# Optimization experiments

Measured on AMD Instinct MI355X. Metric: run time of the kernel, lower is better.

The kernel has to match this reference:

```python
import jax, jax.numpy as jnp
import numpy as np

N_NODES = 50000
N_EDGES = 800000
N_GRAPHS = 256
D_FEAT = 96
HIDDEN = 32


def setup_inputs() -> dict:
    key = jax.random.key(0)
    ks = jax.random.split(key, 8)
    x = jax.random.normal(ks[0], (N_NODES, D_FEAT), dtype=jnp.float32)
    edge_index = jax.random.randint(ks[1], (2, N_EDGES), 0, N_NODES, dtype=jnp.int64)
    batch = jnp.sort(jax.random.randint(ks[2], (N_NODES,), 0, N_GRAPHS, dtype=jnp.int64))
    W1 = jax.random.normal(ks[3], (D_FEAT, HIDDEN), dtype=jnp.float32) * 0.05
    b1 = jnp.zeros((HIDDEN,), dtype=jnp.float32)
    W2 = jax.random.normal(ks[4], (HIDDEN, HIDDEN), dtype=jnp.float32) * 0.05
    b2 = jnp.zeros((HIDDEN,), dtype=jnp.float32)
    Wc = jax.random.normal(ks[5], (HIDDEN, 2), dtype=jnp.float32) * 0.05
    bc = jnp.zeros((2,), dtype=jnp.float32)
    return {"x": x, "edge_index": edge_index, "batch": batch,
            "W1": W1, "b1": b1, "W2": W2, "b2": b2, "Wc": Wc, "bc": bc}


def reference(x, edge_index, batch, W1, b1, W2, b2, Wc, bc):
    src, dst = edge_index[0], edge_index[1]
    # GIN aggregation (eps=0): h_i = x_i + sum_{j -> i} x_j, scatter-add over edges
    agg = jax.ops.segment_sum(x[src], dst, num_segments=N_NODES)
    h = agg + x
    # 2-layer MLP inside GINConv
    h = jnp.maximum(h @ W1 + b1, 0.0) @ W2 + b2
    # outer ReLU (F.relu in forward)
    h = jnp.maximum(h, 0.0)
    # global mean pool per graph
    sums = jax.ops.segment_sum(h, batch, num_segments=N_GRAPHS)          # [G, H]
    counts = jax.ops.segment_sum(jnp.ones((N_NODES,), h.dtype), batch,
                                 num_segments=N_GRAPHS)                   # [G]
    pooled = sums / jnp.maximum(counts, 1.0)[:, None]
    return pooled @ Wc + bc  # [G, 2]
```

## Files before the change

kernel.cpp:

```cpp
#include <hip/hip_runtime.h>
#include <hip/hip_fp16.h>

#define N_NODES 50000
#define N_EDGES 800000
#define N_GRAPHS 256
#define D_FEAT 96
#define HIDDEN 32

#define NB 196
#define PB 500
#define PCHUNK 1600
#define SEGCAP 32
#define NLOAD 16
#define GWIN 16
#define LCAP 6400
#define XT 64
#define XBLK 782
#define XS_STRIDE 97
#define DUMMY_NODE N_NODES

__global__ void __launch_bounds__(256)
k_part(const int* __restrict__ src, const int* __restrict__ dst,
       unsigned int* __restrict__ binned, unsigned short* __restrict__ cnt) {
    __shared__ int hcur[NB];
    int blk = blockIdx.x;
    int tid = threadIdx.x;
    for (int i = tid; i < NB; i += 256) hcur[i] = 0;
    __syncthreads();

    int e0 = blk * PCHUNK, e1 = e0 + PCHUNK;
    for (int it = 0; it < PCHUNK; it += 1024) {
        int e = e0 + it + tid * 4;
        if (e < e1) {
            int4 s4 = *(const int4*)&src[e];
            int4 d4 = *(const int4*)&dst[e];
            unsigned w0 = (unsigned)s4.x | ((unsigned)(d4.x & 255) << 16);
            unsigned w1 = (unsigned)s4.y | ((unsigned)(d4.y & 255) << 16);
            unsigned w2 = (unsigned)s4.z | ((unsigned)(d4.z & 255) << 16);
            unsigned w3 = (unsigned)s4.w | ((unsigned)(d4.w & 255) << 16);
            int b0 = d4.x >> 8, b1 = d4.y >> 8, b2 = d4.z >> 8, b3 = d4.w >> 8;
            int p0 = atomicAdd(&hcur[b0], 1);
            int p1 = atomicAdd(&hcur[b1], 1);
            int p2 = atomicAdd(&hcur[b2], 1);
            int p3 = atomicAdd(&hcur[b3], 1);
            if (p0 < SEGCAP) binned[((size_t)b0 * PB + blk) * SEGCAP + p0] = w0;
            if (p1 < SEGCAP) binned[((size_t)b1 * PB + blk) * SEGCAP + p1] = w1;
            if (p2 < SEGCAP) binned[((size_t)b2 * PB + blk) * SEGCAP + p2] = w2;
            if (p3 < SEGCAP) binned[((size_t)b3 * PB + blk) * SEGCAP + p3] = w3;
        }
    }
    __syncthreads();

    for (int i = tid; i < NB; i += 256) {
        int c = hcur[i]; if (c > SEGCAP) c = SEGCAP;
        cnt[i * PB + blk] = (unsigned short)c;
    }
}

__global__ void __launch_bounds__(256)
k_x(const float* __restrict__ x, const float* __restrict__ W1,
    __half* __restrict__ y16, float* __restrict__ sums,
    float* __restrict__ counts) {
    __shared__ float xs[XT * XS_STRIDE];
    int xb = blockIdx.x;
    int tid = threadIdx.x;
    int n0 = xb * XT;
    int nn = N_NODES - n0; if (nn > XT) nn = XT;

    int gid = xb * 256 + tid;
    if (gid < N_GRAPHS * HIDDEN) sums[gid] = 0.f;
    if (gid < N_GRAPHS) counts[gid] = 0.f;
    if (xb == 0 && tid < HIDDEN)
        y16[(size_t)DUMMY_NODE * HIDDEN + tid] = __float2half(0.f);

    const float4* xsrc = (const float4*)(x + (size_t)n0 * D_FEAT);
    int nf4 = nn * (D_FEAT / 4);
    for (int idx = tid; idx < nf4; idx += 256) {
        int ln = (idx * 2731) >> 16;
        int k4 = idx - ln * 24;
        float4 v = xsrc[idx];
        float* dp = &xs[ln * XS_STRIDE + k4 * 4];
        dp[0] = v.x; dp[1] = v.y; dp[2] = v.z; dp[3] = v.w;
    }
    __syncthreads();

    int lane = tid & 63;
    int f0 = (tid >> 6) << 3;
    f0 = __builtin_amdgcn_readfirstlane(f0);

    if (lane < nn) {
        const float* xr = &xs[lane * XS_STRIDE];
        const float4* W1v = (const float4*)W1;
        float acc[8];
#pragma unroll
        for (int j = 0; j < 8; ++j) acc[j] = 0.f;
#pragma unroll
        for (int k = 0; k < D_FEAT; ++k) {
            float xv = xr[k];
            float4 wa = W1v[k * 8 + (f0 >> 2)];
            float4 wb = W1v[k * 8 + (f0 >> 2) + 1];
            acc[0] = fmaf(xv, wa.x, acc[0]);
            acc[1] = fmaf(xv, wa.y, acc[1]);
            acc[2] = fmaf(xv, wa.z, acc[2]);
            acc[3] = fmaf(xv, wa.w, acc[3]);
            acc[4] = fmaf(xv, wb.x, acc[4]);
            acc[5] = fmaf(xv, wb.y, acc[5]);
            acc[6] = fmaf(xv, wb.z, acc[6]);
            acc[7] = fmaf(xv, wb.w, acc[7]);
        }
        __half2 h01 = __floats2half2_rn(acc[0], acc[1]);
        __half2 h23 = __floats2half2_rn(acc[2], acc[3]);
        __half2 h45 = __floats2half2_rn(acc[4], acc[5]);
        __half2 h67 = __floats2half2_rn(acc[6], acc[7]);
        float4 pack;
        pack.x = __uint_as_float(*(const unsigned*)&h01);
        pack.y = __uint_as_float(*(const unsigned*)&h23);
        pack.z = __uint_as_float(*(const unsigned*)&h45);
        pack.w = __uint_as_float(*(const unsigned*)&h67);
        *(float4*)&y16[(size_t)(n0 + lane) * HIDDEN + f0] = pack;
    }
}

__global__ void __launch_bounds__(1024)
k_agg(const unsigned int* __restrict__ binned, const unsigned short* __restrict__ cnt,
      const __half* __restrict__ y16, const int* __restrict__ batch,
      const float* __restrict__ b1, const float* __restrict__ W2,
      const float* __restrict__ b2,
      float* __restrict__ sums, float* __restrict__ counts) {
    __shared__ unsigned int list[LCAP];
    __shared__ unsigned short list2[LCAP];
    __shared__ unsigned int sA[512], sB[512];
    __shared__ unsigned short cs[PB];
    __shared__ unsigned int sOfs[PB];
    __shared__ unsigned int ncnt[256];
    __shared__ unsigned int offs[257];
    __shared__ unsigned int cur[256];
    __shared__ float w2s[HIDDEN * HIDDEN];
    __shared__ float accs[GWIN * HIDDEN];
    __shared__ float cntsl[GWIN];

    int tid = threadIdx.x;
    int bin = blockIdx.x;
    if (tid < 256) ncnt[tid] = 0;
    w2s[tid] = W2[tid];
    if (tid < GWIN * HIDDEN) accs[tid] = 0.f;
    if (tid < GWIN) cntsl[tid] = 0.f;
    if (tid < 512) {
        unsigned c = (tid < PB) ? (unsigned)cnt[bin * PB + tid] : 0u;
        if (tid < PB) cs[tid] = (unsigned short)c;
        sA[tid] = c;
    }

    const unsigned int* ebase = binned + (size_t)bin * PB * SEGCAP;
    unsigned u[NLOAD];
#pragma unroll
    for (int j = 0; j < NLOAD; ++j)
        u[j] = ebase[tid + j * 1024];
    __syncthreads();

    unsigned *ps = sA, *pd = sB;
    for (int d = 1; d < 512; d <<= 1) {
        if (tid < 512) { unsigned v = ps[tid]; if (tid >= d) v += ps[tid - d]; pd[tid] = v; }
        __syncthreads();
        unsigned* t = ps; ps = pd; pd = t;
    }
    if (tid < PB) sOfs[tid] = tid ? ps[tid - 1] : 0u;
    int ecount = (int)ps[PB - 1];
    if (ecount > LCAP) ecount = LCAP;
    __syncthreads();

#pragma unroll
    for (int j = 0; j < NLOAD; ++j) {
        int idx = tid + j * 1024;
        if (idx < PB * SEGCAP) {
            int s = idx >> 5;
            int i = idx & 31;
            if (i < (int)cs[s]) {
                unsigned pos = sOfs[s] + i;
                if (pos < LCAP) list[pos] = u[j];
            }
        }
    }
    __syncthreads();

    for (int e = tid; e < ecount; e += 1024)
        atomicAdd(&ncnt[list[e] >> 16], 1u);
    __syncthreads();

    if (tid < 256) sA[tid] = (ncnt[tid] + 7u) & ~7u;
    __syncthreads();
    ps = sA; pd = sB;
    for (int d = 1; d < 256; d <<= 1) {
        if (tid < 256) { unsigned v = ps[tid]; if (tid >= d) v += ps[tid - d]; pd[tid] = v; }
        __syncthreads();
        unsigned* t = ps; ps = pd; pd = t;
    }
    if (tid < 256) {
        offs[tid + 1] = ps[tid];
        cur[tid] = tid ? ps[tid - 1] : 0u;
    }
    if (tid == 0) offs[0] = 0;
    __syncthreads();

    for (int e = tid; e < ecount; e += 1024) {
        unsigned p = list[e];
        unsigned pos = atomicAdd(&cur[p >> 16], 1u);
        if (pos < LCAP) list2[pos] = (unsigned short)(p & 0xFFFFu);
    }
    __syncthreads();
    if (tid < 256) {
        unsigned i0 = cur[tid], i1 = offs[tid + 1];
        for (unsigned i = i0; i < i1 && i < LCAP; ++i)
            list2[i] = (unsigned short)DUMMY_NODE;
    }
    __syncthreads();

    int node0 = bin << 8;
    int nn = N_NODES - node0; if (nn > 256) nn = 256;
    int g = tid >> 5;
    int f = tid & 31;
    int gfirst = batch[node0];

    for (int ln = g * 8; ln < g * 8 + 8; ++ln) {
        if (ln >= nn) break;
        int node = node0 + ln;
        float acc = __half2float(y16[(size_t)node * HIDDEN + f]);
        int j = offs[ln], jend = offs[ln + 1];
        for (; j < jend; j += 8) {
            ushort4 qa = *(const ushort4*)&list2[j];
            ushort4 qb = *(const ushort4*)&list2[j + 4];
            float a0 = __half2float(y16[(size_t)qa.x * HIDDEN + f]);
            float a1 = __half2float(y16[(size_t)qa.y * HIDDEN + f]);
            float a2 = __half2float(y16[(size_t)qa.z * HIDDEN + f]);
            float a3 = __half2float(y16[(size_t)qa.w * HIDDEN + f]);
            float a4 = __half2float(y16[(size_t)qb.x * HIDDEN + f]);
            float a5 = __half2float(y16[(size_t)qb.y * HIDDEN + f]);
            float a6 = __half2float(y16[(size_t)qb.z * HIDDEN + f]);
            float a7 = __half2float(y16[(size_t)qb.w * HIDDEN + f]);
            acc += ((a0 + a1) + (a2 + a3)) + ((a4 + a5) + (a6 + a7));
        }

        float h1 = fmaxf(acc + b1[f], 0.f);
        float h2 = b2[f];
#pragma unroll
        for (int k = 0; k < HIDDEN; ++k)
            h2 = fmaf(__shfl(h1, k, 32), w2s[k * HIDDEN + f], h2);
        float h = fmaxf(h2, 0.f);

        int gr = batch[node];
        int b = gr - gfirst;
        if (b < GWIN) {
            atomicAdd(&accs[b * HIDDEN + f], h);
            if (f == 0) atomicAdd(&cntsl[b], 1.f);
        } else {
            atomicAdd(&sums[(size_t)gr * HIDDEN + f], h);
            if (f == 0) atomicAdd(&counts[gr], 1.f);
        }
    }
    __syncthreads();

    for (int i = tid; i < GWIN * HIDDEN; i += 1024) {
        float v = accs[i];
        if (v != 0.f) atomicAdd(&sums[(size_t)gfirst * HIDDEN + i], v);
    }
    if (tid < GWIN) {
        float c = cntsl[tid];
        if (c != 0.f) atomicAdd(&counts[gfirst + tid], c);
    }
}

__global__ void k_out(const float* __restrict__ sums, const float* __restrict__ counts,
                      const float* __restrict__ Wc, const float* __restrict__ bc,
                      float* __restrict__ out) {
    int g = threadIdx.x;
    if (g >= N_GRAPHS) return;
    float inv = 1.f / fmaxf(counts[g], 1.f);
    float o0 = bc[0], o1 = bc[1];
#pragma unroll
    for (int k = 0; k < HIDDEN; ++k) {
        float p = sums[(size_t)g * HIDDEN + k] * inv;
        o0 = fmaf(p, Wc[k * 2 + 0], o0);
        o1 = fmaf(p, Wc[k * 2 + 1], o1);
    }
    out[g * 2 + 0] = o0;
    out[g * 2 + 1] = o1;
}

extern "C" void kernel_launch(void* const* d_in, const int* in_sizes, int n_in,
                              void* d_out, int out_size, void* d_ws, size_t ws_size,
                              hipStream_t stream) {
    const float* x     = (const float*)d_in[0];
    const int*   ei    = (const int*)d_in[1];
    const int*   batch = (const int*)d_in[2];
    const float* W1    = (const float*)d_in[3];
    const float* b1    = (const float*)d_in[4];
    const float* W2    = (const float*)d_in[5];
    const float* b2    = (const float*)d_in[6];
    const float* Wc    = (const float*)d_in[7];
    const float* bc    = (const float*)d_in[8];
    float* out = (float*)d_out;

    char* ws = (char*)d_ws;
    float*          sums   = (float*)ws;
    float*          counts = (float*)(ws + 32768);
    unsigned short* cnt    = (unsigned short*)(ws + 33792);
    unsigned int*   binned = (unsigned int*)(ws + 230400);
    __half*         y16    = (__half*)(ws + 12774400);

    k_part<<<PB, 256, 0, stream>>>(ei, ei + N_EDGES, binned, cnt);

    k_x<<<XBLK, 256, 0, stream>>>(x, W1, y16, sums, counts);

    k_agg<<<NB, 1024, 0, stream>>>(binned, cnt, y16, batch,
                                   b1, W2, b2, sums, counts);

    k_out<<<1, 256, 0, stream>>>(sums, counts, Wc, bc, out);
}
```

Baseline: 131.9 us.

## Merge partition and projection kernels; fold output head into aggregation via ticket

Fuses the edge-partitioning and node-projection kernels into one launch, with each block branching on its index to do one role, so both run concurrently. The final classifier kernel is removed: the last k_agg block to finish, detected through an atomic ticket after a threadfence, computes the pooled outputs. This cuts two kernel launches and lets the two independent front stages overlap. In exchange it adds a serialized tail on one block and a shared-memory union sized for the larger role.

```diff
diff --git a/kernel.cpp b/kernel.cpp
--- a/kernel.cpp
+++ b/kernel.cpp
@@ -20,104 +20,106 @@
 #define DUMMY_NODE N_NODES
 
 __global__ void __launch_bounds__(256)
-k_part(const int* __restrict__ src, const int* __restrict__ dst,
-       unsigned int* __restrict__ binned, unsigned short* __restrict__ cnt) {
-    __shared__ int hcur[NB];
+k_front(const float* __restrict__ x, const float* __restrict__ W1,
+        __half* __restrict__ y16,
+        const int* __restrict__ src, const int* __restrict__ dst,
+        unsigned int* __restrict__ binned, unsigned short* __restrict__ cnt,
+        float* __restrict__ sums, float* __restrict__ counts,
+        unsigned int* __restrict__ ticket) {
+    __shared__ __align__(16) char smem[26656];
     int blk = blockIdx.x;
     int tid = threadIdx.x;
-    for (int i = tid; i < NB; i += 256) hcur[i] = 0;
-    __syncthreads();
-
-    int e0 = blk * PCHUNK, e1 = e0 + PCHUNK;
-    for (int it = 0; it < PCHUNK; it += 1024) {
-        int e = e0 + it + tid * 4;
-        if (e < e1) {
-            int4 s4 = *(const int4*)&src[e];
-            int4 d4 = *(const int4*)&dst[e];
-            unsigned w0 = (unsigned)s4.x | ((unsigned)(d4.x & 255) << 16);
-            unsigned w1 = (unsigned)s4.y | ((unsigned)(d4.y & 255) << 16);
-            unsigned w2 = (unsigned)s4.z | ((unsigned)(d4.z & 255) << 16);
-            unsigned w3 = (unsigned)s4.w | ((unsigned)(d4.w & 255) << 16);
-            int b0 = d4.x >> 8, b1 = d4.y >> 8, b2 = d4.z >> 8, b3 = d4.w >> 8;
-            int p0 = atomicAdd(&hcur[b0], 1);
-            int p1 = atomicAdd(&hcur[b1], 1);
-            int p2 = atomicAdd(&hcur[b2], 1);
-            int p3 = atomicAdd(&hcur[b3], 1);
-            if (p0 < SEGCAP) binned[((size_t)b0 * PB + blk) * SEGCAP + p0] = w0;
-            if (p1 < SEGCAP) binned[((size_t)b1 * PB + blk) * SEGCAP + p1] = w1;
-            if (p2 < SEGCAP) binned[((size_t)b2 * PB + blk) * SEGCAP + p2] = w2;
-            if (p3 < SEGCAP) binned[((size_t)b3 * PB + blk) * SEGCAP + p3] = w3;
-        }
-    }
-    __syncthreads();
-
-    for (int i = tid; i < NB; i += 256) {
-        int c = hcur[i]; if (c > SEGCAP) c = SEGCAP;
-        cnt[i * PB + blk] = (unsigned short)c;
-    }
-}
-
-__global__ void __launch_bounds__(256)
-k_x(const float* __restrict__ x, const float* __restrict__ W1,
-    __half* __restrict__ y16, float* __restrict__ sums,
-    float* __restrict__ counts) {
-    __shared__ float xs[XT * XS_STRIDE];
-    int xb = blockIdx.x;
-    int tid = threadIdx.x;
-    int n0 = xb * XT;
-    int nn = N_NODES - n0; if (nn > XT) nn = XT;
-
-    int gid = xb * 256 + tid;
-    if (gid < N_GRAPHS * HIDDEN) sums[gid] = 0.f;
-    if (gid < N_GRAPHS) counts[gid] = 0.f;
-    if (xb == 0 && tid < HIDDEN)
-        y16[(size_t)DUMMY_NODE * HIDDEN + tid] = __float2half(0.f);
-
-    const float4* xsrc = (const float4*)(x + (size_t)n0 * D_FEAT);
-    int nf4 = nn * (D_FEAT / 4);
-    for (int idx = tid; idx < nf4; idx += 256) {
-        int ln = (idx * 2731) >> 16;
-        int k4 = idx - ln * 24;
-        float4 v = xsrc[idx];
-        float* dp = &xs[ln * XS_STRIDE + k4 * 4];
-        dp[0] = v.x; dp[1] = v.y; dp[2] = v.z; dp[3] = v.w;
-    }
-    __syncthreads();
-
-    int lane = tid & 63;
-    int f0 = (tid >> 6) << 3;
-    f0 = __builtin_amdgcn_readfirstlane(f0);
-
-    if (lane < nn) {
-        const float* xr = &xs[lane * XS_STRIDE];
-        const float4* W1v = (const float4*)W1;
-        float acc[8];
-#pragma unroll
-        for (int j = 0; j < 8; ++j) acc[j] = 0.f;
-#pragma unroll
-        for (int k = 0; k < D_FEAT; ++k) {
-            float xv = xr[k];
-            float4 wa = W1v[k * 8 + (f0 >> 2)];
-            float4 wb = W1v[k * 8 + (f0 >> 2) + 1];
-            acc[0] = fmaf(xv, wa.x, acc[0]);
-            acc[1] = fmaf(xv, wa.y, acc[1]);
-            acc[2] = fmaf(xv, wa.z, acc[2]);
-            acc[3] = fmaf(xv, wa.w, acc[3]);
-            acc[4] = fmaf(xv, wb.x, acc[4]);
-            acc[5] = fmaf(xv, wb.y, acc[5]);
-            acc[6] = fmaf(xv, wb.z, acc[6]);
-            acc[7] = fmaf(xv, wb.w, acc[7]);
-        }
-        __half2 h01 = __floats2half2_rn(acc[0], acc[1]);
-        __half2 h23 = __floats2half2_rn(acc[2], acc[3]);
-        __half2 h45 = __floats2half2_rn(acc[4], acc[5]);
-        __half2 h67 = __floats2half2_rn(acc[6], acc[7]);
-        float4 pack;
-        pack.x = __uint_as_float(*(const unsigned*)&h01);
-        pack.y = __uint_as_float(*(const unsigned*)&h23);
-        pack.z = __uint_as_float(*(const unsigned*)&h45);
-        pack.w = __uint_as_float(*(const unsigned*)&h67);
-        *(float4*)&y16[(size_t)(n0 + lane) * HIDDEN + f0] = pack;
+    if (blk < PB) {
+        int* hcur = (int*)smem;
+        for (int i = tid; i < NB; i += 256) hcur[i] = 0;
+        __syncthreads();
+
+        int e0 = blk * PCHUNK, e1 = e0 + PCHUNK;
+        for (int it = 0; it < PCHUNK; it += 1024) {
+            int e = e0 + it + tid * 4;
+            if (e < e1) {
+                int4 s4 = *(const int4*)&src[e];
+                int4 d4 = *(const int4*)&dst[e];
+                unsigned w0 = (unsigned)s4.x | ((unsigned)(d4.x & 255) << 16);
+                unsigned w1 = (unsigned)s4.y | ((unsigned)(d4.y & 255) << 16);
+                unsigned w2 = (unsigned)s4.z | ((unsigned)(d4.z & 255) << 16);
+                unsigned w3 = (unsigned)s4.w | ((unsigned)(d4.w & 255) << 16);
+                int b0 = d4.x >> 8, b1 = d4.y >> 8, b2 = d4.z >> 8, b3 = d4.w >> 8;
+                int p0 = atomicAdd(&hcur[b0], 1);
+                int p1 = atomicAdd(&hcur[b1], 1);
+                int p2 = atomicAdd(&hcur[b2], 1);
+                int p3 = atomicAdd(&hcur[b3], 1);
+                if (p0 < SEGCAP) binned[((size_t)b0 * PB + blk) * SEGCAP + p0] = w0;
+                if (p1 < SEGCAP) binned[((size_t)b1 * PB + blk) * SEGCAP + p1] = w1;
+                if (p2 < SEGCAP) binned[((size_t)b2 * PB + blk) * SEGCAP + p2] = w2;
+                if (p3 < SEGCAP) binned[((size_t)b3 * PB + blk) * SEGCAP + p3] = w3;
+            }
+        }
+        __syncthreads();
+
+        for (int i = tid; i < NB; i += 256) {
+            int c = hcur[i]; if (c > SEGCAP) c = SEGCAP;
+            cnt[i * PB + blk] = (unsigned short)c;
+        }
+    } else {
+        float* xs = (float*)smem;
+        int xb = blk - PB;
+        int n0 = xb * XT;
+        int nn = N_NODES - n0; if (nn > XT) nn = XT;
+
+        int gid = xb * 256 + tid;
+        if (gid < N_GRAPHS * HIDDEN) sums[gid] = 0.f;
+        if (gid < N_GRAPHS) counts[gid] = 0.f;
+        if (xb == 0 && tid == 0) *ticket = 0u;
+        if (xb == 0 && tid < HIDDEN)
+            y16[(size_t)DUMMY_NODE * HIDDEN + tid] = __float2half(0.f);
+
+        const float4* xsrc = (const float4*)(x + (size_t)n0 * D_FEAT);
+        int nf4 = nn * (D_FEAT / 4);
+        for (int idx = tid; idx < nf4; idx += 256) {
+            int ln = (idx * 2731) >> 16;
+            int k4 = idx - ln * 24;
+            float4 v = xsrc[idx];
+            float* dp = &xs[ln * XS_STRIDE + k4 * 4];
+            dp[0] = v.x; dp[1] = v.y; dp[2] = v.z; dp[3] = v.w;
+        }
+        __syncthreads();
+
+        int lane = tid & 63;
+        int f0 = (tid >> 6) << 3;
+        f0 = __builtin_amdgcn_readfirstlane(f0);
+
+        if (lane < nn) {
+            const float* xr = &xs[lane * XS_STRIDE];
+            const float4* W1v = (const float4*)W1;
+            float acc[8];
+#pragma unroll
+            for (int j = 0; j < 8; ++j) acc[j] = 0.f;
+#pragma unroll
+            for (int k = 0; k < D_FEAT; ++k) {
+                float xv = xr[k];
+                float4 wa = W1v[k * 8 + (f0 >> 2)];
+                float4 wb = W1v[k * 8 + (f0 >> 2) + 1];
+                acc[0] = fmaf(xv, wa.x, acc[0]);
+                acc[1] = fmaf(xv, wa.y, acc[1]);
+                acc[2] = fmaf(xv, wa.z, acc[2]);
+                acc[3] = fmaf(xv, wa.w, acc[3]);
+                acc[4] = fmaf(xv, wb.x, acc[4]);
+                acc[5] = fmaf(xv, wb.y, acc[5]);
+                acc[6] = fmaf(xv, wb.z, acc[6]);
+                acc[7] = fmaf(xv, wb.w, acc[7]);
+            }
+            __half2 h01 = __floats2half2_rn(acc[0], acc[1]);
+            __half2 h23 = __floats2half2_rn(acc[2], acc[3]);
+            __half2 h45 = __floats2half2_rn(acc[4], acc[5]);
+            __half2 h67 = __floats2half2_rn(acc[6], acc[7]);
+            float4 pack;
+            pack.x = __uint_as_float(*(const unsigned*)&h01);
+            pack.y = __uint_as_float(*(const unsigned*)&h23);
+            pack.z = __uint_as_float(*(const unsigned*)&h45);
+            pack.w = __uint_as_float(*(const unsigned*)&h67);
+            *(float4*)&y16[(size_t)(n0 + lane) * HIDDEN + f0] = pack;
+        }
     }
 }
 
@@ -125,8 +127,10 @@
 k_agg(const unsigned int* __restrict__ binned, const unsigned short* __restrict__ cnt,
       const __half* __restrict__ y16, const int* __restrict__ batch,
       const float* __restrict__ b1, const float* __restrict__ W2,
-      const float* __restrict__ b2,
-      float* __restrict__ sums, float* __restrict__ counts) {
+      const float* __restrict__ b2, const float* __restrict__ Wc,
+      const float* __restrict__ bc,
+      float* __restrict__ sums, float* __restrict__ counts,
+      unsigned int* __restrict__ ticket, float* __restrict__ out) {
     __shared__ unsigned int list[LCAP];
     __shared__ unsigned short list2[LCAP];
     __shared__ unsigned int sA[512], sB[512];
@@ -138,6 +142,7 @@
     __shared__ float w2s[HIDDEN * HIDDEN];
     __shared__ float accs[GWIN * HIDDEN];
     __shared__ float cntsl[GWIN];
+    __shared__ unsigned int lastFlag;
 
     int tid = threadIdx.x;
     int bin = blockIdx.x;
@@ -267,23 +272,25 @@
         float c = cntsl[tid];
         if (c != 0.f) atomicAdd(&counts[gfirst + tid], c);
     }
-}
-
-__global__ void k_out(const float* __restrict__ sums, const float* __restrict__ counts,
-                      const float* __restrict__ Wc, const float* __restrict__ bc,
-                      float* __restrict__ out) {
-    int g = threadIdx.x;
-    if (g >= N_GRAPHS) return;
-    float inv = 1.f / fmaxf(counts[g], 1.f);
-    float o0 = bc[0], o1 = bc[1];
-#pragma unroll
-    for (int k = 0; k < HIDDEN; ++k) {
-        float p = sums[(size_t)g * HIDDEN + k] * inv;
-        o0 = fmaf(p, Wc[k * 2 + 0], o0);
-        o1 = fmaf(p, Wc[k * 2 + 1], o1);
-    }
-    out[g * 2 + 0] = o0;
-    out[g * 2 + 1] = o1;
+
+    __threadfence();
+    if (tid == 0)
+        lastFlag = (atomicAdd(ticket, 1u) == (unsigned)(NB - 1)) ? 1u : 0u;
+    __syncthreads();
+    if (lastFlag && tid < N_GRAPHS) {
+        int gr = tid;
+        float c = atomicAdd(&counts[gr], 0.f);
+        float inv = 1.f / fmaxf(c, 1.f);
+        float o0 = bc[0], o1 = bc[1];
+#pragma unroll
+        for (int k = 0; k < HIDDEN; ++k) {
+            float p = atomicAdd(&sums[(size_t)gr * HIDDEN + k], 0.f) * inv;
+            o0 = fmaf(p, Wc[k * 2 + 0], o0);
+            o1 = fmaf(p, Wc[k * 2 + 1], o1);
+        }
+        out[gr * 2 + 0] = o0;
+        out[gr * 2 + 1] = o1;
+    }
 }
 
 extern "C" void kernel_launch(void* const* d_in, const int* in_sizes, int n_in,
@@ -303,16 +310,15 @@
     char* ws = (char*)d_ws;
     float*          sums   = (float*)ws;
     float*          counts = (float*)(ws + 32768);
-    unsigned short* cnt    = (unsigned short*)(ws + 33792);
-    unsigned int*   binned = (unsigned int*)(ws + 230400);
-    __half*         y16    = (__half*)(ws + 12774400);
-
-    k_part<<<PB, 256, 0, stream>>>(ei, ei + N_EDGES, binned, cnt);
-
-    k_x<<<XBLK, 256, 0, stream>>>(x, W1, y16, sums, counts);
+    unsigned int*   ticket = (unsigned int*)(ws + 33792);
+    unsigned short* cnt    = (unsigned short*)(ws + 33808);
+    unsigned int*   binned = (unsigned int*)(ws + 229808);
+    __half*         y16    = (__half*)(ws + 12773808);
+
+    k_front<<<PB + XBLK, 256, 0, stream>>>(
+        x, W1, y16, ei, ei + N_EDGES, binned, cnt, sums, counts, ticket);
 
     k_agg<<<NB, 1024, 0, stream>>>(binned, cnt, y16, batch,
-                                   b1, W2, b2, sums, counts);
-
-    k_out<<<1, 256, 0, stream>>>(sums, counts, Wc, bc, out);
+                                   b1, W2, b2, Wc, bc,
+                                   sums, counts, ticket, out);
 }
```

After: 183.8 us. +39.4%, slower.
